# Optimization experiments

Measured on AMD Instinct MI355X. Metric: run time of the kernel, lower is better.

Reference implementation:

```python
import math
import jax, jax.numpy as jnp
import numpy as np

B, S, D, H = 2, 2048, 1024, 16
HD = D // H  # 64


def setup_inputs() -> dict:
    key = jax.random.key(0)
    k = jax.random.split(key, 8)
    x = jax.random.normal(k[0], (B, S, D), dtype=jnp.float32)
    # RoPE tables: inv_freq over half dim, emb = concat(freqs, freqs)
    inv_freq = 1.0 / (10000.0 ** (jnp.arange(0, HD, 2, dtype=jnp.float32) / HD))
    pos = jnp.arange(S, dtype=jnp.float32)
    freqs = pos[:, None] * inv_freq[None, :]            # [S, HD/2]
    emb = jnp.concatenate([freqs, freqs], axis=-1)      # [S, HD]
    cos = jnp.cos(emb)[:, None, :]                      # [S, 1, HD] broadcasts over [B,S,H,HD]
    sin = jnp.sin(emb)[:, None, :]
    # causal additive mask [1, 1, S, S]
    neg = jnp.finfo(jnp.float32).min
    mask = jnp.where(jnp.tril(jnp.ones((S, S), dtype=bool)), 0.0, neg)[None, None]
    scale = 0.02
    wq = jax.random.normal(k[1], (D, D), dtype=jnp.float32) * scale
    wk = jax.random.normal(k[2], (D, D), dtype=jnp.float32) * scale
    wv = jax.random.normal(k[3], (D, D), dtype=jnp.float32) * scale
    wo = jax.random.normal(k[4], (D, D), dtype=jnp.float32) * scale
    return {"x": x, "cos": cos, "sin": sin, "mask": mask,
            "wq": wq, "wk": wk, "wv": wv, "wo": wo}


def rotate_half(t):
    t1, t2 = t[..., : t.shape[-1] // 2], t[..., t.shape[-1] // 2:]
    return jnp.concatenate([-t2, t1], axis=-1)


def reference(x, cos, sin, mask, wq, wk, wv, wo):
    b, s, d = x.shape
    # torch nn.Linear: y = x @ W^T  (W is [out, in])
    q = (x @ wq.T).reshape(b, s, H, HD)
    kk = (x @ wk.T).reshape(b, s, H, HD)
    v = (x @ wv.T).reshape(b, s, H, HD)
    q = q * cos + rotate_half(q) * sin
    kk = kk * cos + rotate_half(kk) * sin
    q = q.transpose(0, 2, 1, 3)   # [b, h, s, hd]
    kk = kk.transpose(0, 2, 1, 3)
    v = v.transpose(0, 2, 1, 3)
    scores = jnp.einsum('bhqd,bhkd->bhqk', q, kk) / math.sqrt(HD)
    scores = scores + mask
    probs = jax.nn.softmax(scores.astype(jnp.float32), axis=-1).astype(q.dtype)
    out = jnp.einsum('bhqk,bhkd->bhqd', probs, v)
    out = out.transpose(0, 2, 1, 3).reshape(b, s, d)
    return out @ wo.T
```

## Files before the change

kernel.cpp:

```cpp
#include <hip/hip_runtime.h>
#include <hip/hip_bf16.h>

typedef __hip_bfloat16 bf16;
typedef unsigned short u16;
typedef __attribute__((ext_vector_type(8))) short short8;
typedef __attribute__((ext_vector_type(4))) float floatx4;

constexpr int B_ = 2, S_ = 2048, D_ = 1024, H_ = 16, HD_ = 64;
constexpr int KT = 64, PAD = 72;
constexpr int GK = 1024, BK = 64;

__device__ inline float b2f(u16 u) {
    union { unsigned int i; float f; } v; v.i = ((unsigned int)u) << 16; return v.f;
}
__device__ inline u16 f2b(float f) {
    bf16 h = __float2bfloat16(f); return *(u16*)&h;
}

__device__ inline void gl16(const u16* g, u16* l) {
    __builtin_amdgcn_global_load_lds(
        (const __attribute__((address_space(1))) unsigned int*)g,
        (__attribute__((address_space(3))) unsigned int*)l, 16, 0, 0);
}

#define SBAR() __builtin_amdgcn_sched_barrier(0)

__global__ __launch_bounds__(256) void cvt_kernel(
    const float* __restrict__ x,  const float* __restrict__ wq,
    const float* __restrict__ wk, const float* __restrict__ wv,
    const float* __restrict__ wo,
    u16* __restrict__ Xb, u16* __restrict__ Wb)
{
    const size_t c = (size_t)blockIdx.x * 256 + threadIdx.x;
    const float* src; u16* dst; size_t off;
    if (c < (size_t)(1 << 19)) { src = x; dst = Xb; off = c; }
    else {
        const size_t w = c - (1 << 19);
        const int wi = (int)(w >> 17);
        off = w & ((1 << 17) - 1);
        src = (wi == 0) ? wq : (wi == 1) ? wk : (wi == 2) ? wv : wo;
        dst = Wb + ((size_t)wi << 20);
    }
    const float4 a = *(const float4*)(src + off * 8);
    const float4 b = *(const float4*)(src + off * 8 + 4);
    ushort4 u0; u0.x = f2b(a.x); u0.y = f2b(a.y); u0.z = f2b(a.z); u0.w = f2b(a.w);
    ushort4 u1; u1.x = f2b(b.x); u1.y = f2b(b.y); u1.z = f2b(b.z); u1.w = f2b(b.w);
    *(ushort4*)(dst + off * 8)     = u0;
    *(ushort4*)(dst + off * 8 + 4) = u1;
}

__global__ __launch_bounds__(512, 2) void qkv8(
    const u16* __restrict__ Ag, const u16* __restrict__ Wall,
    const float* __restrict__ cosp, const float* __restrict__ sinp,
    bf16* __restrict__ Qo, bf16* __restrict__ Ko, u16* __restrict__ Vt)
{
    extern __shared__ u16 lds[];

    const int wgid = (blockIdx.x & 7) * 24 + (blockIdx.x >> 3);
    const int mt = wgid / 12;
    const int rem = wgid - mt * 12;
    const int nt = rem & 3, z = rem >> 2;

    const u16* W = Wall + ((size_t)z << 20);
    const int m0 = mt * 256, n0 = nt * 256;

    const int tid  = threadIdx.x;
    const int wave = tid >> 6, lane = tid & 63;
    const int quad = lane >> 4, l16 = lane & 15;
    const int wm = wave >> 2, wn = wave & 3;

    const int lr_st = wave * 16 + (lane >> 2);
    const int csrc  = ((lane & 3) ^ ((lane >> 5) << 1)) * 8;
    const int grA   = ((lr_st >> 6) << 7) + (lr_st & 63);
    const int grB   = ((lr_st >> 5) << 6) + (lr_st & 31);

    const int cidx = ((quad ^ (((l16 >> 3) & 1) << 1))) * 8;

    floatx4 acc[8][4] = {};
    short8 af[4][2], bA[2][2], bB[2][2];

    const u16* A_st = Ag + (size_t)(m0 + grA) * GK + csrc;
    const u16* B_st = W  + (size_t)(n0 + grB) * GK + csrc;

    auto stA = [&](int t2, int mh) {
        if (t2 > 15) return;
        const u16* s = A_st + ((size_t)mh * 64) * GK + t2 * 64;
        u16* d = lds + (((t2 & 1) * 2 + mh) * 8192) + wave * 512;
        gl16(s, d);
        gl16(s + 32, d + 4096);
    };
    auto stB = [&](int t2, int nh) {
        if (t2 > 15) return;
        const u16* s = B_st + ((size_t)nh * 32) * GK + t2 * 64;
        u16* d = lds + 32768 + (((t2 & 1) * 2 + nh) * 8192) + wave * 512;
        gl16(s, d);
        gl16(s + 32, d + 4096);
    };
    auto rdA = [&](int sl, int mh) {
        const int base = (sl * 2 + mh) * 8192 + cidx;
#pragma unroll
        for (int mf = 0; mf < 4; ++mf) {
            const int lr = wm * 64 + mf * 16 + l16;
#pragma unroll
            for (int ks = 0; ks < 2; ++ks)
                af[mf][ks] = *(const short8*)&lds[base + ks * 4096 + lr * 32];
        }
    };
    auto rdB = [&](short8 (&bf)[2][2], int sl, int nh) {
        const int base = 32768 + (sl * 2 + nh) * 8192 + cidx;
#pragma unroll
        for (int fn = 0; fn < 2; ++fn) {
            const int lr = wn * 32 + fn * 16 + l16;
#pragma unroll
            for (int ks = 0; ks < 2; ++ks)
                bf[fn][ks] = *(const short8*)&lds[base + ks * 4096 + lr * 32];
        }
    };
    auto mm = [&](int mh, int nh, short8 (&bf)[2][2]) {
#pragma unroll
        for (int mf = 0; mf < 4; ++mf)
#pragma unroll
            for (int fn = 0; fn < 2; ++fn)
#pragma unroll
                for (int ks = 0; ks < 2; ++ks)
                    acc[mh * 4 + mf][nh * 2 + fn] =
                        __builtin_amdgcn_mfma_f32_16x16x32_bf16(
                            af[mf][ks], bf[fn][ks],
                            acc[mh * 4 + mf][nh * 2 + fn], 0, 0, 0);
    };

    stA(0, 0); stB(0, 0); stA(0, 1); stB(0, 1); stA(1, 0); stB(1, 0);
    asm volatile("s_waitcnt vmcnt(4)" ::: "memory");
    SBAR(); __builtin_amdgcn_s_barrier(); SBAR();

    for (int t = 0; t < 16; ++t) {
        const int sl = t & 1;
        rdA(sl, 0); rdB(bA, sl, 0); stA(t + 1, 1);
        mm(0, 0, bA);
        rdB(bB, sl, 1); stB(t + 1, 1);
        mm(0, 1, bB);
        rdA(sl, 1); stA(t + 2, 0);
        mm(1, 0, bA);
        stB(t + 2, 0);
        mm(1, 1, bB);
        SBAR();
        if (t < 14)       asm volatile("s_waitcnt vmcnt(4)" ::: "memory");
        else if (t == 14) asm volatile("s_waitcnt vmcnt(0)" ::: "memory");
        __builtin_amdgcn_s_barrier();
        SBAR();
    }

    const int s0 = m0 & (S_ - 1);
    const int bq = m0 >> 11;
    const int h  = (n0 >> 6) + wn;

    if (z < 2) {
        float* Cs = (float*)lds;
        float* Sn = (float*)(lds + 16384);
        {
            const int rr = tid >> 1;
            const int cc = (tid & 1) * 16;
            const float4* cp = (const float4*)(cosp + (size_t)(s0 + rr) * HD_ + cc);
            const float4* sp = (const float4*)(sinp + (size_t)(s0 + rr) * HD_ + cc);
            float4* cd = (float4*)&Cs[rr * 32 + cc];
            float4* sd = (float4*)&Sn[rr * 32 + cc];
            cd[0] = cp[0]; cd[1] = cp[1]; cd[2] = cp[2]; cd[3] = cp[3];
            sd[0] = sp[0]; sd[1] = sp[1]; sd[2] = sp[2]; sd[3] = sp[3];
        }
        __syncthreads();

        const float scale = (z == 0) ? 0.125f * 1.44269504f : 1.0f;
        bf16* C = (z == 0) ? Qo : Ko;
#pragma unroll
        for (int mf = 0; mf < 8; ++mf)
#pragma unroll
            for (int r = 0; r < 4; ++r) {
                const int mr = wm * 128 + mf * 16 + quad * 4 + r;
                const size_t base = ((size_t)(bq * H_ + h) * S_ + s0 + mr) << 6;
#pragma unroll
                for (int np = 0; np < 2; ++np) {
                    const int d = np * 16 + l16;
                    const float c1 = Cs[mr * 32 + d];
                    const float s1 = Sn[mr * 32 + d];
                    const float q0 = acc[mf][np][r], q1 = acc[mf][np + 2][r];
                    C[base + d]      = __float2bfloat16((q0 * c1 - q1 * s1) * scale);
                    C[base + d + 32] = __float2bfloat16((q1 * c1 + q0 * s1) * scale);
                }
            }
    } else {
        const int bh = bq * H_ + h;
#pragma unroll
        for (int mf = 0; mf < 8; ++mf)
#pragma unroll
            for (int nf = 0; nf < 4; ++nf) {
                const int hd = nf * 16 + l16;
                const int sb = s0 + wm * 128 + mf * 16 + quad * 4;
                ushort4 pk;
                pk.x = f2b(acc[mf][nf][0]); pk.y = f2b(acc[mf][nf][1]);
                pk.z = f2b(acc[mf][nf][2]); pk.w = f2b(acc[mf][nf][3]);
                *(ushort4*)&Vt[((size_t)(bh * HD_ + hd) << 11) + sb] = pk;
            }
    }
}

template <typename TC, int SCATTER, int ROPE, int BN>
__global__ __launch_bounds__(256) void gemm_async(
    const u16* __restrict__ A, const u16* __restrict__ Wb,
    const float* __restrict__ cosp, const float* __restrict__ sinp,
    TC* __restrict__ C0, TC* __restrict__ C1, TC* __restrict__ C2, int N)
{
    constexpr int NT = BN / 32;

    int x, y, z;
    {
        const int xcd = blockIdx.x & 7, idx = blockIdx.x >> 3;
        y = (xcd & 3) * 8 + (idx & 7);
        if (BN == 128) {
            const int xz = (xcd >> 2) * 12 + (idx >> 3);
            x = xz & 7; z = xz >> 3;
        } else {
            x = (xcd >> 2) * 8 + (idx >> 3);
            z = 0;
        }
    }

    const u16* W = Wb + ((size_t)z << 20);
    TC*        C = (z == 0) ? C0 : (z == 1 ? C1 : C2);

    __shared__ __align__(16) u16 As[128 * BK];
    __shared__ __align__(16) u16 Bs[BN * BK];

    const int tid  = threadIdx.x;
    const int wave = tid >> 6, lane = tid & 63;
    const int quad = lane >> 4, l16 = lane & 15;
    const int wm = wave >> 1, wn = wave & 1;
    const int m0 = y * 128, n0 = x * BN;

    const int srl = lane >> 3;
    const int sc  = (lane & 7) ^ srl;

    floatx4 acc[4][NT] = {};

    for (int k0 = 0; k0 < GK; k0 += BK) {
        __syncthreads();
#pragma unroll
        for (int j = 0; j < 4; ++j) {
            const int rb = wave * 32 + j * 8;
            gl16(A + (size_t)(m0 + rb + srl) * GK + k0 + sc * 8, &As[rb * BK]);
        }
#pragma unroll
        for (int j = 0; j < BN / 32; ++j) {
            const int rb = wave * (BN / 4) + j * 8;
            gl16(W + (size_t)(n0 + rb + srl) * GK + k0 + sc * 8, &Bs[rb * BK]);
        }
        __syncthreads();

#pragma unroll
        for (int ks = 0; ks < 2; ++ks) {
            short8 af[4], bfr[NT];
#pragma unroll
            for (int mt = 0; mt < 4; ++mt) {
                const int R = wm * 64 + mt * 16 + l16;
                af[mt] = *(const short8*)&As[R * BK + (((ks * 4 + quad) ^ (l16 & 7)) * 8)];
            }
#pragma unroll
            for (int nt = 0; nt < NT; ++nt) {
                const int R = wn * (BN / 2) + nt * 16 + l16;
                bfr[nt] = *(const short8*)&Bs[R * BK + (((ks * 4 + quad) ^ (l16 & 7)) * 8)];
            }
#pragma unroll
            for (int mt = 0; mt < 4; ++mt)
#pragma unroll
                for (int nt = 0; nt < NT; ++nt)
                    acc[mt][nt] = __builtin_amdgcn_mfma_f32_16x16x32_bf16(
                        af[mt], bfr[nt], acc[mt][nt], 0, 0, 0);
        }
    }

    {
#pragma unroll
        for (int mt = 0; mt < 4; ++mt)
#pragma unroll
            for (int nt = 0; nt < NT; ++nt)
#pragma unroll
                for (int r = 0; r < 4; ++r) {
                    const int m = m0 + wm * 64 + mt * 16 + quad * 4 + r;
                    const int n = n0 + wn * (BN / 2) + nt * 16 + l16;
                    ((float*)C)[(size_t)m * N + n] = acc[mt][nt][r];
                }
    }
}

__global__ __launch_bounds__(256, 4) void fa_kernel(
    const u16* __restrict__ Qg, const u16* __restrict__ Kg, const u16* __restrict__ Vt,
    bf16* __restrict__ Og)
{
    __shared__ __align__(16) u16 Kt[2][KT * PAD];
    __shared__ __align__(16) u16 Vs[2][KT * PAD];

    const int flat = blockIdx.x;
    const int bh = flat & 31;
    const int rk = flat >> 5;
    const int g  = rk >> 3, j = rk & 7;
    const int qt = (g == 0) ? 31 - j : (g == 1) ? j : (g == 2) ? 23 - j : 8 + j;
    const int b  = bh >> 4, h = bh & 15;
    const int tid  = threadIdx.x;
    const int wave = tid >> 6, lane = tid & 63;
    const int quad = lane >> 4, l16 = lane & 15;
    const int srow = tid >> 2;
    const int sc4  = tid & 3;
    const int scol = sc4 * 16;
    const int vwb  = (sc4 >> 1) * 32 + (sc4 & 1) * 4;

    const int qrow0 = qt * 64 + wave * 16;

    union S8U { short8 v; ushort4 q[2]; };

    short8 aq0, aq1;
    {
        const u16* qrow = Qg + ((size_t)bh * S_ + qrow0 + l16) * HD_;
        aq0 = *(const short8*)(qrow + quad * 8);
        aq1 = *(const short8*)(qrow + 32 + quad * 8);
    }

    floatx4 oacc[4] = {};
    float lsum = 0.f;

    const int T = qt + 1;

    {
        const u16* kp = Kg + ((size_t)bh * S_ + srow) * HD_ + scol;
        *(short8*)&Kt[0][srow * PAD + scol]     = *(const short8*)kp;
        *(short8*)&Kt[0][srow * PAD + scol + 8] = *(const short8*)(kp + 8);
        const u16* vp = Vt + ((size_t)bh * HD_ + srow) * S_ + scol;
        S8U v0, v1; v0.v = *(const short8*)vp; v1.v = *(const short8*)(vp + 8);
        *(ushort4*)&Vs[0][srow * PAD + vwb]      = v0.q[0];
        *(ushort4*)&Vs[0][srow * PAD + vwb + 8]  = v0.q[1];
        *(ushort4*)&Vs[0][srow * PAD + vwb + 16] = v1.q[0];
        *(ushort4*)&Vs[0][srow * PAD + vwb + 24] = v1.q[1];
    }
    __syncthreads();

    for (int it = 0; it < T; ++it) {
        const int  cur = it & 1;
        const bool pf  = (it + 1 < T);
        short8 nk0, nk1; S8U nv0, nv1;
        if (pf) {
            const int kb2 = (it + 1) * KT;
            const u16* kp = Kg + ((size_t)bh * S_ + kb2 + srow) * HD_ + scol;
            nk0 = *(const short8*)kp; nk1 = *(const short8*)(kp + 8);
            const u16* vp = Vt + ((size_t)bh * HD_ + srow) * S_ + kb2 + scol;
            nv0.v = *(const short8*)vp; nv1.v = *(const short8*)(vp + 8);
        }

        floatx4 s0[4] = {{0,0,0,0},{0,0,0,0},{0,0,0,0},{0,0,0,0}};
        __builtin_amdgcn_s_setprio(1);
#pragma unroll
        for (int kt = 0; kt < 4; ++kt) {
            const short8 bk0 = *(const short8*)&Kt[cur][(kt * 16 + l16) * PAD + quad * 8];
            const short8 bk1 = *(const short8*)&Kt[cur][(kt * 16 + l16) * PAD + 32 + quad * 8];
            s0[kt] = __builtin_amdgcn_mfma_f32_16x16x32_bf16(bk0, aq0, s0[kt], 0, 0, 0);
            s0[kt] = __builtin_amdgcn_mfma_f32_16x16x32_bf16(bk1, aq1, s0[kt], 0, 0, 0);
        }
        __builtin_amdgcn_s_setprio(0);

        if (it == T - 1) {
            const int t0 = wave * 16 + l16 - quad * 4;
#pragma unroll
            for (int kt = 0; kt < 4; ++kt)
#pragma unroll
                for (int r = 0; r < 4; ++r)
                    if (kt * 16 + r > t0) s0[kt][r] = -1.0e38f;
        }

        short8 ah0, ah1;
        float rs = 0.f;
#pragma unroll
        for (int kt = 0; kt < 4; ++kt)
#pragma unroll
            for (int r = 0; r < 4; ++r) {
                const float e0 = __builtin_amdgcn_exp2f(s0[kt][r]);
                rs += e0;
                const int idx = (kt & 1) * 4 + r;
                if (kt < 2) ah0[idx] = (short)f2b(e0);
                else        ah1[idx] = (short)f2b(e0);
            }
        lsum += rs;

        __builtin_amdgcn_s_setprio(1);
#pragma unroll
        for (int dt = 0; dt < 4; ++dt) {
            const short8 bv0 = *(const short8*)&Vs[cur][(dt * 16 + l16) * PAD + quad * 8];
            const short8 bv1 = *(const short8*)&Vs[cur][(dt * 16 + l16) * PAD + 32 + quad * 8];
            oacc[dt] = __builtin_amdgcn_mfma_f32_16x16x32_bf16(bv0, ah0, oacc[dt], 0, 0, 0);
            oacc[dt] = __builtin_amdgcn_mfma_f32_16x16x32_bf16(bv1, ah1, oacc[dt], 0, 0, 0);
        }
        __builtin_amdgcn_s_setprio(0);

        if (pf) {
            const int nb = cur ^ 1;
            *(short8*)&Kt[nb][srow * PAD + scol]     = nk0;
            *(short8*)&Kt[nb][srow * PAD + scol + 8] = nk1;
            *(ushort4*)&Vs[nb][srow * PAD + vwb]      = nv0.q[0];
            *(ushort4*)&Vs[nb][srow * PAD + vwb + 8]  = nv0.q[1];
            *(ushort4*)&Vs[nb][srow * PAD + vwb + 16] = nv1.q[0];
            *(ushort4*)&Vs[nb][srow * PAD + vwb + 24] = nv1.q[1];
        }
        __syncthreads();
    }

    lsum += __shfl_xor(lsum, 16);
    lsum += __shfl_xor(lsum, 32);
    const float inv = 1.0f / lsum;
    bf16* orow = Og + ((size_t)(b * S_ + qrow0 + l16)) * D_ + h * HD_;
#pragma unroll
    for (int dt = 0; dt < 4; ++dt) {
        ushort4 pk;
        pk.x = f2b(oacc[dt][0] * inv);
        pk.y = f2b(oacc[dt][1] * inv);
        pk.z = f2b(oacc[dt][2] * inv);
        pk.w = f2b(oacc[dt][3] * inv);
        *(ushort4*)((u16*)orow + dt * 16 + quad * 4) = pk;
    }
}

extern "C" void kernel_launch(void* const* d_in, const int* in_sizes, int n_in,
                              void* d_out, int out_size, void* d_ws, size_t ws_size,
                              hipStream_t stream)
{
    const float* x    = (const float*)d_in[0];
    const float* cosp = (const float*)d_in[1];
    const float* sinp = (const float*)d_in[2];
    const float* wq   = (const float*)d_in[4];
    const float* wk   = (const float*)d_in[5];
    const float* wv   = (const float*)d_in[6];
    const float* wo   = (const float*)d_in[7];
    float* out = (float*)d_out;

    u16* w0 = (u16*)d_ws;
    const size_t NE = (size_t)B_ * S_ * D_;
    u16* Qb  = w0;
    u16* Kb  = w0 + NE;
    u16* Vtb = w0 + 2 * NE;
    u16* Xb  = w0 + 3 * NE;
    u16* Wb  = w0 + 4 * NE;
    u16* Ab  = Xb;
    u16* Wob = Wb + 3 * (1 << 20);

    static bool inited = false;
    if (!inited) {
        hipFuncSetAttribute((const void*)qkv8,
                            hipFuncAttributeMaxDynamicSharedMemorySize, 131072);
        inited = true;
    }

    cvt_kernel<<<4096, 256, 0, stream>>>(x, wq, wk, wv, wo, Xb, Wb);

    qkv8<<<192, 512, 131072, stream>>>(
        Xb, Wb, cosp, sinp, (bf16*)Qb, (bf16*)Kb, Vtb);

    fa_kernel<<<1024, 256, 0, stream>>>(Qb, Kb, Vtb, (bf16*)Ab);

    gemm_async<float, 0, 0, 64><<<512, 256, 0, stream>>>(
        Ab, Wob, cosp, sinp, out, out, out, D_);
}
```

Before: 173.9 us.

## Load QKV GEMM weight fragments directly to registers, bypassing LDS

The weight (B) operand in the QKV projection GEMM is no longer staged through LDS. Each wave loads its MFMA fragments directly from global memory into double-buffered registers one k-step ahead, while A stays in LDS. The loop is restructured into unrolled ping-pong iterations with adjusted waitcnts, and dynamic shared memory is halved. This removes LDS writes and reads for B but adds redundant, less coalesced global loads and more register pressure.

```diff
diff --git a/kernel.cpp b/kernel.cpp
--- a/kernel.cpp
+++ b/kernel.cpp
@@ -72,29 +72,31 @@
     const int lr_st = wave * 16 + (lane >> 2);
     const int csrc  = ((lane & 3) ^ ((lane >> 5) << 1)) * 8;
     const int grA   = ((lr_st >> 6) << 7) + (lr_st & 63);
-    const int grB   = ((lr_st >> 5) << 6) + (lr_st & 31);
 
     const int cidx = ((quad ^ (((l16 >> 3) & 1) << 1))) * 8;
 
     floatx4 acc[8][4] = {};
-    short8 af[4][2], bA[2][2], bB[2][2];
-
-    const u16* A_st = Ag + (size_t)(m0 + grA) * GK + csrc;
-    const u16* B_st = W  + (size_t)(n0 + grB) * GK + csrc;
+    short8 af[4][2];
+    short8 BA[2][2][2], BB[2][2][2];
+
+    const u16* A_st  = Ag + (size_t)(m0 + grA) * GK + csrc;
+    const u16* Brow  = W  + (size_t)(n0 + wn * 64 + l16) * GK + quad * 8;
 
     auto stA = [&](int t2, int mh) {
-        if (t2 > 15) return;
         const u16* s = A_st + ((size_t)mh * 64) * GK + t2 * 64;
         u16* d = lds + (((t2 & 1) * 2 + mh) * 8192) + wave * 512;
         gl16(s, d);
         gl16(s + 32, d + 4096);
     };
-    auto stB = [&](int t2, int nh) {
-        if (t2 > 15) return;
-        const u16* s = B_st + ((size_t)nh * 32) * GK + t2 * 64;
-        u16* d = lds + 32768 + (((t2 & 1) * 2 + nh) * 8192) + wave * 512;
-        gl16(s, d);
-        gl16(s + 32, d + 4096);
+    auto ldB = [&](int t2, short8 (&Bf)[2][2][2]) {
+#pragma unroll
+        for (int nh = 0; nh < 2; ++nh)
+#pragma unroll
+            for (int fn = 0; fn < 2; ++fn)
+#pragma unroll
+                for (int ks = 0; ks < 2; ++ks)
+                    Bf[nh][fn][ks] = *(const short8*)(
+                        Brow + (size_t)(nh * 32 + fn * 16) * GK + t2 * 64 + ks * 32);
     };
     auto rdA = [&](int sl, int mh) {
         const int base = (sl * 2 + mh) * 8192 + cidx;
@@ -106,17 +108,7 @@
                 af[mf][ks] = *(const short8*)&lds[base + ks * 4096 + lr * 32];
         }
     };
-    auto rdB = [&](short8 (&bf)[2][2], int sl, int nh) {
-        const int base = 32768 + (sl * 2 + nh) * 8192 + cidx;
-#pragma unroll
-        for (int fn = 0; fn < 2; ++fn) {
-            const int lr = wn * 32 + fn * 16 + l16;
-#pragma unroll
-            for (int ks = 0; ks < 2; ++ks)
-                bf[fn][ks] = *(const short8*)&lds[base + ks * 4096 + lr * 32];
-        }
-    };
-    auto mm = [&](int mh, int nh, short8 (&bf)[2][2]) {
+    auto mm = [&](int mh, int nh, short8 (&Bf)[2][2][2]) {
 #pragma unroll
         for (int mf = 0; mf < 4; ++mf)
 #pragma unroll
@@ -125,30 +117,37 @@
                 for (int ks = 0; ks < 2; ++ks)
                     acc[mh * 4 + mf][nh * 2 + fn] =
                         __builtin_amdgcn_mfma_f32_16x16x32_bf16(
-                            af[mf][ks], bf[fn][ks],
+                            af[mf][ks], Bf[nh][fn][ks],
                             acc[mh * 4 + mf][nh * 2 + fn], 0, 0, 0);
     };
 
-    stA(0, 0); stB(0, 0); stA(0, 1); stB(0, 1); stA(1, 0); stB(1, 0);
-    asm volatile("s_waitcnt vmcnt(4)" ::: "memory");
+    stA(0, 0); stA(0, 1); ldB(0, BA);
+    asm volatile("s_waitcnt vmcnt(8)" ::: "memory");
     SBAR(); __builtin_amdgcn_s_barrier(); SBAR();
 
-    for (int t = 0; t < 16; ++t) {
-        const int sl = t & 1;
-        rdA(sl, 0); rdB(bA, sl, 0); stA(t + 1, 1);
-        mm(0, 0, bA);
-        rdB(bB, sl, 1); stB(t + 1, 1);
-        mm(0, 1, bB);
-        rdA(sl, 1); stA(t + 2, 0);
-        mm(1, 0, bA);
-        stB(t + 2, 0);
-        mm(1, 1, bB);
-        SBAR();
-        if (t < 14)       asm volatile("s_waitcnt vmcnt(4)" ::: "memory");
-        else if (t == 14) asm volatile("s_waitcnt vmcnt(0)" ::: "memory");
-        __builtin_amdgcn_s_barrier();
-        SBAR();
-    }
+#define QKV_BODY(T, CUR, NXT)                                        \
+    {                                                                \
+        const int sl = (T) & 1;                                      \
+        stA((T) + 1, 0); stA((T) + 1, 1);       \
+        ldB((T) + 1, NXT);                                           \
+        rdA(sl, 0); mm(0, 0, CUR); mm(0, 1, CUR);                    \
+        rdA(sl, 1); mm(1, 0, CUR); mm(1, 1, CUR);                    \
+        SBAR();                                                      \
+        asm volatile("s_waitcnt vmcnt(8)" ::: "memory");             \
+        __builtin_amdgcn_s_barrier(); SBAR();                        \
+    }
+
+    for (int tt = 0; tt < 7; ++tt) {
+        QKV_BODY(2 * tt,     BA, BB);
+        QKV_BODY(2 * tt + 1, BB, BA);
+    }
+    QKV_BODY(14, BA, BB);
+    {
+        rdA(1, 0); mm(0, 0, BB); mm(0, 1, BB);
+        rdA(1, 1); mm(1, 0, BB); mm(1, 1, BB);
+        SBAR(); __builtin_amdgcn_s_barrier(); SBAR();
+    }
+#undef QKV_BODY
 
     const int s0 = m0 & (S_ - 1);
     const int bq = m0 >> 11;
@@ -450,13 +449,13 @@
     static bool inited = false;
     if (!inited) {
         hipFuncSetAttribute((const void*)qkv8,
-                            hipFuncAttributeMaxDynamicSharedMemorySize, 131072);
+                            hipFuncAttributeMaxDynamicSharedMemorySize, 65536);
         inited = true;
     }
 
     cvt_kernel<<<4096, 256, 0, stream>>>(x, wq, wk, wv, wo, Xb, Wb);
 
-    qkv8<<<192, 512, 131072, stream>>>(
+    qkv8<<<192, 512, 65536, stream>>>(
         Xb, Wb, cosp, sinp, (bf16*)Qb, (bf16*)Kb, Vtb);
 
     fa_kernel<<<1024, 256, 0, stream>>>(Qb, Kb, Vtb, (bf16*)Ab);
```

Measured after the change: 189.2 us. 8.8% more time.
